# Kernel optimization log

Measured on AMD Instinct MI355X. Metric: run time of the kernel, lower is better.

Reference implementation:

```python
import jax, jax.numpy as jnp
import numpy as np

K = 20  # kNN fan-out


def knn_idx(x, k):
    # x: (B, C, N). Negative squared pairwise distance; top-k largest = nearest.
    inner = -2.0 * jnp.einsum('bcn,bcm->bnm', x, x)        # (B, N, N)
    xx = jnp.sum(x * x, axis=1)                            # (B, N)
    pd = -xx[:, :, None] - inner - xx[:, None, :]          # (B, N, N)
    return jax.lax.top_k(pd, k)[1]                         # (B, N, k) int32


def get_graph_feature(x, k):
    # x: (B, C, N) -> edge features (B, 2C, N, k)
    idx = knn_idx(x, k)                                    # (B, N, k)
    xt = jnp.transpose(x, (0, 2, 1))                       # (B, N, C)
    nbrs = jax.vmap(lambda pts, ids: pts[ids])(xt, idx)    # (B, N, k, C)
    center = xt[:, :, None, :]                             # (B, N, 1, C)
    feat = jnp.concatenate(
        [nbrs - center, jnp.broadcast_to(center, nbrs.shape)], axis=-1)  # (B,N,k,2C)
    return jnp.transpose(feat, (0, 3, 1, 2))               # (B, 2C, N, k)


def vn_layer(W, x):
    # W: (out, in); x: (B, in, N, k) -> (B, out, N, k)
    return jnp.einsum('oi,bink->bonk', W, x)


def setup_inputs() -> dict:
    key = jax.random.key(0)
    ks = jax.random.split(key, 6)
    B, C, N = 16, 3, 2048
    num_classes = 10
    return {
        'x': jax.random.normal(ks[0], (B, C, N), dtype=jnp.float32),
        'W1': jax.random.normal(ks[1], (64, 6), dtype=jnp.float32),
        'W2': jax.random.normal(ks[2], (128, 64), dtype=jnp.float32),
        'W3': jax.random.normal(ks[3], (256, 128), dtype=jnp.float32),
        'fc_w': jax.random.normal(ks[4], (num_classes, 256), dtype=jnp.float32) * 0.0625,
        'fc_b': jax.random.normal(ks[5], (num_classes,), dtype=jnp.float32) * 0.0625,
    }


def reference(x, W1, W2, W3, fc_w, fc_b):
    h = get_graph_feature(x, K)          # (B, 6, N, k)
    h = vn_layer(W1, h)                  # (B, 64, N, k)
    h = jax.nn.relu(vn_layer(W2, h))     # (B, 128, N, k)
    h = jax.nn.relu(vn_layer(W3, h))     # (B, 256, N, k)
    h = jnp.max(h, axis=-1)              # max over neighbors k -> (B, 256, N)
    h = jnp.max(h, axis=-1)              # global max over points -> (B, 256)
    return h @ fc_w.T + fc_b             # (B, num_classes)
```

## Files before the change

### kernel.cpp

```cpp
#include <hip/hip_runtime.h>
#include <stdint.h>

typedef _Float16 v8h __attribute__((ext_vector_type(8)));
typedef _Float16 v2h __attribute__((ext_vector_type(2)));
typedef float v4f __attribute__((ext_vector_type(4)));
typedef float v16f __attribute__((ext_vector_type(16)));

#define NPTS 2048
#define BATCH 16
#define KNN 20
#define PAIRS (NPTS * KNN)

__device__ __forceinline__ unsigned pair_relu_h2(unsigned pu, unsigned qu) {
  v2h a = *(const v2h*)&pu;
  v2h b = *(const v2h*)&qu;
  v2h s = a + b;
  v2h z = {(_Float16)0.f, (_Float16)0.f};
  v2h r = __builtin_elementwise_max(s, z);
  return *(const unsigned*)&r;
}
__device__ __forceinline__ float fmax3(float a, float b, float c) {
  return fmaxf(fmaxf(a, b), c);
}

__global__ void prep_kernel(const float* __restrict__ W1, const float* __restrict__ W2,
                            float* __restrict__ M2a, float* __restrict__ M2b,
                            int* __restrict__ H) {
  if (blockIdx.x == 0 && threadIdx.x < 128) {
    int o = threadIdx.x;
    float a0 = 0, a1 = 0, a2 = 0, b0 = 0, b1 = 0, b2 = 0;
    for (int i = 0; i < 64; ++i) {
      float w2 = W2[o * 64 + i];
      const float* w1r = W1 + i * 6;
      a0 += w2 * w1r[0]; a1 += w2 * w1r[1]; a2 += w2 * w1r[2];
      b0 += w2 * (w1r[3] - w1r[0]); b1 += w2 * (w1r[4] - w1r[1]); b2 += w2 * (w1r[5] - w1r[2]);
    }
    M2a[o * 3 + 0] = a0; M2a[o * 3 + 1] = a1; M2a[o * 3 + 2] = a2;
    M2b[o * 3 + 0] = b0; M2b[o * 3 + 1] = b1; M2b[o * 3 + 2] = b2;
  }
  int g = blockIdx.x * 128 + threadIdx.x;
  if (g < BATCH * 256) H[g] = 0;
}

__global__ __launch_bounds__(64) void pq_kernel(const float* __restrict__ x,
                                                const float* __restrict__ M2a,
                                                const float* __restrict__ M2b,
                                                unsigned short* __restrict__ p,
                                                unsigned short* __restrict__ q) {
  int b = blockIdx.x >> 6;
  int j0 = (blockIdx.x & 63) << 5;
  int t = threadIdx.x;
  int o0 = t * 2;
  float a00 = M2a[o0 * 3 + 0], a01 = M2a[o0 * 3 + 1], a02 = M2a[o0 * 3 + 2];
  float a10 = M2a[o0 * 3 + 3], a11 = M2a[o0 * 3 + 4], a12 = M2a[o0 * 3 + 5];
  float b00 = M2b[o0 * 3 + 0], b01 = M2b[o0 * 3 + 1], b02 = M2b[o0 * 3 + 2];
  float b10 = M2b[o0 * 3 + 3], b11 = M2b[o0 * 3 + 4], b12 = M2b[o0 * 3 + 5];
  const float* xb = x + b * 3 * NPTS;
  unsigned* pw = (unsigned*)p;
  unsigned* qw = (unsigned*)q;
  for (int jj = 0; jj < 32; ++jj) {
    int j = j0 + jj;
    float x0 = xb[j], x1 = xb[NPTS + j], x2 = xb[2 * NPTS + j];
    float p0 = a00 * x0 + a01 * x1 + a02 * x2;
    float p1 = a10 * x0 + a11 * x1 + a12 * x2;
    float q0 = b00 * x0 + b01 * x1 + b02 * x2;
    float q1 = b10 * x0 + b11 * x1 + b12 * x2;
    size_t base = ((size_t)(b * NPTS + j)) * 64 + t;
    auto hp = __builtin_amdgcn_cvt_pkrtz(p0, p1);
    auto hq = __builtin_amdgcn_cvt_pkrtz(q0, q1);
    pw[base] = *(const unsigned*)&hp;
    qw[base] = *(const unsigned*)&hq;
  }
}

__global__ __launch_bounds__(512, 4) void knn_kernel(const float* __restrict__ x,
                                                     int* __restrict__ idxOut) {
  __shared__ float4 pts[NPTS];
  __shared__ unsigned long long cand[8][8][64];
  int b = blockIdx.x >> 5;
  int qblk = blockIdx.x & 31;
  const float* xb = x + b * 3 * NPTS;
  for (int i = threadIdx.x; i < NPTS; i += 512) {
    float X = xb[i], Y = xb[NPTS + i], Z = xb[2 * NPTS + i];
    pts[i] = make_float4(X, Y, Z, X * X + Y * Y + Z * Z);
  }
  __syncthreads();
  int wid = threadIdx.x >> 6, lane = threadIdx.x & 63;
  int qbase = qblk * 64 + wid * 8;

  float m2x[8], m2y[8], m2z[8], mn[8];
#pragma unroll
  for (int g = 0; g < 8; ++g) {
    float4 qp = pts[qbase + g];
    m2x[g] = -2.f * qp.x; m2y[g] = -2.f * qp.y; m2z[g] = -2.f * qp.z;
    mn[g] = 1e30f;
  }

  for (int s = 0; s < 32; ++s) {
    float4 P = pts[s * 64 + lane];
#pragma unroll
    for (int g = 0; g < 8; ++g) {
      float d = fmaf(m2x[g], P.x, fmaf(m2y[g], P.y, fmaf(m2z[g], P.z, P.w)));
      mn[g] = fminf(mn[g], d);
    }
  }

  float tau[8];
#pragma unroll
  for (int g = 0; g < 8; ++g) {
    float v = mn[g];
    for (int k = 2; k <= 64; k <<= 1) {
      for (int j = k >> 1; j > 0; j >>= 1) {
        float o = __shfl_xor(v, j);
        bool low = (lane & j) == 0;
        bool up = (lane & k) == 0;
        v = (low == up) ? fminf(v, o) : fmaxf(v, o);
      }
    }
    float t = __shfl(v, 19);
    tau[g] = t + fabsf(t) * 4e-6f + 1e-6f;
  }

  int cnt[8] = {0, 0, 0, 0, 0, 0, 0, 0};
  for (int s = 0; s < 32; ++s) {
    int i = s * 64 + lane;
    float4 P = pts[i];
#pragma unroll
    for (int g = 0; g < 8; ++g) {
      float d = fmaf(m2x[g], P.x, fmaf(m2y[g], P.y, fmaf(m2z[g], P.z, P.w)));
      bool take = d <= tau[g];
      unsigned long long mb = __ballot(take);
      if (take) {
        int pos = cnt[g] + __popcll(mb & ((1ull << lane) - 1ull));
        if (pos < 64) {
          unsigned kd = __float_as_uint(d + 64.f);
          cand[wid][g][pos] = (((unsigned long long)kd) << 32) | (unsigned)i;
        }
      }
      cnt[g] += __popcll(mb);
    }
  }

#pragma unroll
  for (int g = 0; g < 8; ++g) {
    int nc = cnt[g] < 64 ? cnt[g] : 64;
    unsigned long long k0 = (lane < nc) ? cand[wid][g][lane] : ~0ull;
    int r0 = 0;
    for (int i = 0; i < nc; ++i) r0 += (cand[wid][g][i] < k0) ? 1 : 0;
    long long obase = ((long long)b * NPTS + qbase + g) * KNN;
    if (lane < nc && r0 < KNN) idxOut[obase + r0] = (int)(k0 & 0xffffffffu);
  }
}

__global__ __launch_bounds__(256, 3) void gemm_max_kernel(
    const unsigned short* __restrict__ p, const unsigned short* __restrict__ q,
    const int* __restrict__ idx, const float* __restrict__ W3, int* __restrict__ H) {
  __shared__ __align__(16) unsigned short h2s[2][32 * 128];

  int b = blockIdx.x & 15;
  int w = blockIdx.x >> 4;
  int t = threadIdx.x;
  int lane = t & 63, wid = t >> 6;
  int col = lane & 31, hi = lane >> 5;

  v8h bfr0[8], bfr1[8];
#pragma unroll
  for (int kk = 0; kk < 8; ++kk) {
    const float* s0 = W3 + (size_t)(wid * 64 + col) * 128 + kk * 16 + hi * 8;
    const float* s1 = s0 + 32 * 128;
    v8h f0, f1;
#pragma unroll
    for (int jj = 0; jj < 8; ++jj) { f0[jj] = (_Float16)s0[jj]; f1[jj] = (_Float16)s1[jj]; }
    bfr0[kk] = f0; bfr1[kk] = f1;
  }

  const unsigned short* pB = p + (size_t)b * NPTS * 128;
  const unsigned short* qB = q + (size_t)b * NPTS * 128;
  const int* idxB = idx + (size_t)b * PAIRS;

  int pm = t >> 3;
  int c2 = t & 7;
  int st0 = pm * 128 + (((c2 * 2) ^ (pm & 7)) * 8);
  int st1 = pm * 128 + (((c2 * 2 + 1) ^ (pm & 7)) * 8);

  const int NT = PAIRS / 32;

  uint4 P0, P1, Q0, Q1;
  int jn = 0;
  {
    int pr = w * 32 + pm;
    int j = idxB[pr] & (NPTS - 1);
    int n = pr / 20;
    P0 = *(const uint4*)(pB + (size_t)j * 128 + c2 * 16);
    P1 = *(const uint4*)(pB + (size_t)j * 128 + c2 * 16 + 8);
    Q0 = *(const uint4*)(qB + (size_t)n * 128 + c2 * 16);
    Q1 = *(const uint4*)(qB + (size_t)n * 128 + c2 * 16 + 8);
    int T1 = w + 64;
    if (T1 < NT) jn = idxB[T1 * 32 + pm];
  }

  float vmx0 = 0.f, vmx1 = 0.f;
  int buf = 0;
  for (int T = w; T < NT; T += 64) {
    uint4 R0, R1;
    R0.x = pair_relu_h2(P0.x, Q0.x); R0.y = pair_relu_h2(P0.y, Q0.y);
    R0.z = pair_relu_h2(P0.z, Q0.z); R0.w = pair_relu_h2(P0.w, Q0.w);
    R1.x = pair_relu_h2(P1.x, Q1.x); R1.y = pair_relu_h2(P1.y, Q1.y);
    R1.z = pair_relu_h2(P1.z, Q1.z); R1.w = pair_relu_h2(P1.w, Q1.w);
    *(uint4*)&h2s[buf][st0] = R0;
    *(uint4*)&h2s[buf][st1] = R1;
    __syncthreads();

    int Tn = T + 64;
    if (Tn < NT) {
      int prn = Tn * 32 + pm;
      int j = jn & (NPTS - 1);
      int n = prn / 20;
      P0 = *(const uint4*)(pB + (size_t)j * 128 + c2 * 16);
      P1 = *(const uint4*)(pB + (size_t)j * 128 + c2 * 16 + 8);
      Q0 = *(const uint4*)(qB + (size_t)n * 128 + c2 * 16);
      Q1 = *(const uint4*)(qB + (size_t)n * 128 + c2 * 16 + 8);
      int T2 = T + 128;
      if (T2 < NT) jn = idxB[T2 * 32 + pm];
    }

    v16f acc0 = {0.f}, acc1 = {0.f};
#pragma unroll
    for (int kk = 0; kk < 8; ++kk) {
      v8h a = *(const v8h*)&h2s[buf][col * 128 + (((kk * 2 + hi) ^ (col & 7)) * 8)];
      acc0 = __builtin_amdgcn_mfma_f32_32x32x16_f16(a, bfr0[kk], acc0, 0, 0, 0);
      acc1 = __builtin_amdgcn_mfma_f32_32x32x16_f16(a, bfr1[kk], acc1, 0, 0, 0);
    }
    {
      float m0 = fmax3(acc0[0], acc0[1], acc0[2]);
      float m1 = fmax3(acc0[3], acc0[4], acc0[5]);
      float m2 = fmax3(acc0[6], acc0[7], acc0[8]);
      float m3 = fmax3(acc0[9], acc0[10], acc0[11]);
      float m4 = fmax3(acc0[12], acc0[13], acc0[14]);
      vmx0 = fmax3(fmax3(m0, m1, m2), fmax3(m3, m4, acc0[15]), vmx0);
      float n0 = fmax3(acc1[0], acc1[1], acc1[2]);
      float n1 = fmax3(acc1[3], acc1[4], acc1[5]);
      float n2 = fmax3(acc1[6], acc1[7], acc1[8]);
      float n3 = fmax3(acc1[9], acc1[10], acc1[11]);
      float n4 = fmax3(acc1[12], acc1[13], acc1[14]);
      vmx1 = fmax3(fmax3(n0, n1, n2), fmax3(n3, n4, acc1[15]), vmx1);
    }
    buf ^= 1;
  }

  float v0 = fmaxf(vmx0, __shfl_xor(vmx0, 32));
  float v1 = fmaxf(vmx1, __shfl_xor(vmx1, 32));
  if (hi == 0) {
    atomicMax(&H[b * 256 + wid * 64 + col], __float_as_int(v0));
    atomicMax(&H[b * 256 + wid * 64 + 32 + col], __float_as_int(v1));
  }
}

__global__ __launch_bounds__(64) void fc_kernel(const int* __restrict__ Hi,
                                                const float* __restrict__ fcw,
                                                const float* __restrict__ fcb,
                                                float* __restrict__ out) {
  int b = blockIdx.x / 10, r = blockIdx.x % 10;
  int lane = threadIdx.x;
  const float* Hb = (const float*)Hi + b * 256;
  float s = 0.f;
#pragma unroll
  for (int c = lane; c < 256; c += 64) s += Hb[c] * fcw[r * 256 + c];
#pragma unroll
  for (int m = 32; m > 0; m >>= 1) s += __shfl_xor(s, m);
  if (lane == 0) out[b * 10 + r] = s + fcb[r];
}

extern "C" void kernel_launch(void* const* d_in, const int* in_sizes, int n_in,
                              void* d_out, int out_size, void* d_ws, size_t ws_size,
                              hipStream_t stream) {
  const float* x   = (const float*)d_in[0];
  const float* W1  = (const float*)d_in[1];
  const float* W2  = (const float*)d_in[2];
  const float* W3  = (const float*)d_in[3];
  const float* fcw = (const float*)d_in[4];
  const float* fcb = (const float*)d_in[5];
  float* out = (float*)d_out;
  char* ws = (char*)d_ws;

  float* M2a = (float*)(ws + 0);
  float* M2b = (float*)(ws + 1536);
  int* H     = (int*)(ws + 4096);
  int* idx   = (int*)(ws + 24576);
  unsigned short* p = (unsigned short*)(ws + 3145728);
  unsigned short* q = (unsigned short*)(ws + 12582912);

  prep_kernel<<<32, 128, 0, stream>>>(W1, W2, M2a, M2b, H);
  pq_kernel<<<BATCH * 64, 64, 0, stream>>>(x, M2a, M2b, p, q);
  knn_kernel<<<BATCH * 32, 512, 0, stream>>>(x, idx);
  gemm_max_kernel<<<BATCH * 64, 256, 0, stream>>>(p, q, idx, W3, H);
  fc_kernel<<<BATCH * 10, 64, 0, stream>>>(H, fcw, fcb, out);
}
```

Measured before the change: 166.7 us.

## Load gathered pair rows directly into MFMA operands, dropping LDS staging and barriers

The gemm_max kernel no longer stages relu(p[j]+q[n]) tiles through double-buffered shared memory with a block-wide sync. Each wave now gathers its own 32 pair rows straight from global memory into registers in MFMA A-fragment layout and applies the add and relu there. Each of the four waves loads the same rows redundantly, and the launch-bounds occupancy hint is removed. This avoids the LDS round-trip and the __syncthreads, but it raises global/L2 traffic and register pressure, and it loses the software prefetch of the next tile's P and Q rows (only the next index is prefetched). The loop is also hard-coded to 20 iterations.

```diff
diff --git a/kernel.cpp b/kernel.cpp
--- a/kernel.cpp
+++ b/kernel.cpp
@@ -152,21 +152,19 @@
   }
 }
 
-__global__ __launch_bounds__(256, 3) void gemm_max_kernel(
+__global__ void gemm_max_kernel(
     const unsigned short* __restrict__ p, const unsigned short* __restrict__ q,
     const int* __restrict__ idx, const float* __restrict__ W3, int* __restrict__ H) {
-  __shared__ __align__(16) unsigned short h2s[2][32 * 128];
-
   int b = blockIdx.x & 15;
-  int w = blockIdx.x >> 4;
+  int tg = blockIdx.x >> 4;
   int t = threadIdx.x;
-  int lane = t & 63, wid = t >> 6;
+  int lane = t & 63, cg = t >> 6;
   int col = lane & 31, hi = lane >> 5;
 
   v8h bfr0[8], bfr1[8];
 #pragma unroll
   for (int kk = 0; kk < 8; ++kk) {
-    const float* s0 = W3 + (size_t)(wid * 64 + col) * 128 + kk * 16 + hi * 8;
+    const float* s0 = W3 + (size_t)(cg * 64 + col) * 128 + kk * 16 + hi * 8;
     const float* s1 = s0 + 32 * 128;
     v8h f0, f1;
 #pragma unroll
@@ -178,81 +176,55 @@
   const unsigned short* qB = q + (size_t)b * NPTS * 128;
   const int* idxB = idx + (size_t)b * PAIRS;
 
-  int pm = t >> 3;
-  int c2 = t & 7;
-  int st0 = pm * 128 + (((c2 * 2) ^ (pm & 7)) * 8);
-  int st1 = pm * 128 + (((c2 * 2 + 1) ^ (pm & 7)) * 8);
-
   const int NT = PAIRS / 32;
-
-  uint4 P0, P1, Q0, Q1;
-  int jn = 0;
-  {
-    int pr = w * 32 + pm;
-    int j = idxB[pr] & (NPTS - 1);
-    int n = pr / 20;
-    P0 = *(const uint4*)(pB + (size_t)j * 128 + c2 * 16);
-    P1 = *(const uint4*)(pB + (size_t)j * 128 + c2 * 16 + 8);
-    Q0 = *(const uint4*)(qB + (size_t)n * 128 + c2 * 16);
-    Q1 = *(const uint4*)(qB + (size_t)n * 128 + c2 * 16 + 8);
-    int T1 = w + 64;
-    if (T1 < NT) jn = idxB[T1 * 32 + pm];
-  }
+  const v8h zero8 = {0, 0, 0, 0, 0, 0, 0, 0};
+
+  int jcur = idxB[tg * 32 + col];
 
   float vmx0 = 0.f, vmx1 = 0.f;
-  int buf = 0;
-  for (int T = w; T < NT; T += 64) {
-    uint4 R0, R1;
-    R0.x = pair_relu_h2(P0.x, Q0.x); R0.y = pair_relu_h2(P0.y, Q0.y);
-    R0.z = pair_relu_h2(P0.z, Q0.z); R0.w = pair_relu_h2(P0.w, Q0.w);
-    R1.x = pair_relu_h2(P1.x, Q1.x); R1.y = pair_relu_h2(P1.y, Q1.y);
-    R1.z = pair_relu_h2(P1.z, Q1.z); R1.w = pair_relu_h2(P1.w, Q1.w);
-    *(uint4*)&h2s[buf][st0] = R0;
-    *(uint4*)&h2s[buf][st1] = R1;
-    __syncthreads();
-
-    int Tn = T + 64;
-    if (Tn < NT) {
-      int prn = Tn * 32 + pm;
-      int j = jn & (NPTS - 1);
-      int n = prn / 20;
-      P0 = *(const uint4*)(pB + (size_t)j * 128 + c2 * 16);
-      P1 = *(const uint4*)(pB + (size_t)j * 128 + c2 * 16 + 8);
-      Q0 = *(const uint4*)(qB + (size_t)n * 128 + c2 * 16);
-      Q1 = *(const uint4*)(qB + (size_t)n * 128 + c2 * 16 + 8);
-      int T2 = T + 128;
-      if (T2 < NT) jn = idxB[T2 * 32 + pm];
+  for (int k = 0; k < 20; ++k) {
+    int T = tg + k * 64;
+    unsigned pr = (unsigned)(T * 32 + col);
+    int j = jcur & (NPTS - 1);
+    unsigned n = pr / 20u;
+    const unsigned short* prow = pB + (size_t)j * 128;
+    const unsigned short* qrow = qB + (size_t)n * 128;
+
+    if (k < 19) jcur = idxB[(T + 64) * 32 + col];
+
+    v8h P[8], Q[8];
+#pragma unroll
+    for (int kk = 0; kk < 8; ++kk) {
+      P[kk] = *(const v8h*)(prow + kk * 16 + hi * 8);
+      Q[kk] = *(const v8h*)(qrow + kk * 16 + hi * 8);
     }
 
     v16f acc0 = {0.f}, acc1 = {0.f};
 #pragma unroll
     for (int kk = 0; kk < 8; ++kk) {
-      v8h a = *(const v8h*)&h2s[buf][col * 128 + (((kk * 2 + hi) ^ (col & 7)) * 8)];
+      v8h a = __builtin_elementwise_max(P[kk] + Q[kk], zero8);
       acc0 = __builtin_amdgcn_mfma_f32_32x32x16_f16(a, bfr0[kk], acc0, 0, 0, 0);
       acc1 = __builtin_amdgcn_mfma_f32_32x32x16_f16(a, bfr1[kk], acc1, 0, 0, 0);
     }
-    {
-      float m0 = fmax3(acc0[0], acc0[1], acc0[2]);
-      float m1 = fmax3(acc0[3], acc0[4], acc0[5]);
-      float m2 = fmax3(acc0[6], acc0[7], acc0[8]);
-      float m3 = fmax3(acc0[9], acc0[10], acc0[11]);
-      float m4 = fmax3(acc0[12], acc0[13], acc0[14]);
-      vmx0 = fmax3(fmax3(m0, m1, m2), fmax3(m3, m4, acc0[15]), vmx0);
-      float n0 = fmax3(acc1[0], acc1[1], acc1[2]);
-      float n1 = fmax3(acc1[3], acc1[4], acc1[5]);
-      float n2 = fmax3(acc1[6], acc1[7], acc1[8]);
-      float n3 = fmax3(acc1[9], acc1[10], acc1[11]);
-      float n4 = fmax3(acc1[12], acc1[13], acc1[14]);
-      vmx1 = fmax3(fmax3(n0, n1, n2), fmax3(n3, n4, acc1[15]), vmx1);
-    }
-    buf ^= 1;
+    float m0 = fmax3(acc0[0], acc0[1], acc0[2]);
+    float m1 = fmax3(acc0[3], acc0[4], acc0[5]);
+    float m2 = fmax3(acc0[6], acc0[7], acc0[8]);
+    float m3 = fmax3(acc0[9], acc0[10], acc0[11]);
+    float m4 = fmax3(acc0[12], acc0[13], acc0[14]);
+    vmx0 = fmax3(fmax3(m0, m1, m2), fmax3(m3, m4, acc0[15]), vmx0);
+    float n0 = fmax3(acc1[0], acc1[1], acc1[2]);
+    float n1 = fmax3(acc1[3], acc1[4], acc1[5]);
+    float n2 = fmax3(acc1[6], acc1[7], acc1[8]);
+    float n3 = fmax3(acc1[9], acc1[10], acc1[11]);
+    float n4 = fmax3(acc1[12], acc1[13], acc1[14]);
+    vmx1 = fmax3(fmax3(n0, n1, n2), fmax3(n3, n4, acc1[15]), vmx1);
   }
 
   float v0 = fmaxf(vmx0, __shfl_xor(vmx0, 32));
   float v1 = fmaxf(vmx1, __shfl_xor(vmx1, 32));
   if (hi == 0) {
-    atomicMax(&H[b * 256 + wid * 64 + col], __float_as_int(v0));
-    atomicMax(&H[b * 256 + wid * 64 + 32 + col], __float_as_int(v1));
+    atomicMax(&H[b * 256 + cg * 64 + col], __float_as_int(v0));
+    atomicMax(&H[b * 256 + cg * 64 + 32 + col], __float_as_int(v1));
   }
 }
 
```

Result: slower. 224.7 us (+34.7%).
